# Optimization experiments

Measured on AMD Instinct MI355X. Metric: run time of the kernel, lower is better.

## Reference

```python
import jax, jax.numpy as jnp
import numpy as np

I, H, O = 256, 1024, 256
B, T = 64, 512


def setup_inputs() -> dict:
    key = jax.random.key(0)
    ks = jax.random.split(key, 7)
    s = 1.0 / np.sqrt(H)
    return {
        "x": jax.random.normal(ks[0], (B, T, I), dtype=jnp.float32),
        "W_ih": jax.random.uniform(ks[1], (4 * H, I), jnp.float32, -s, s),
        "W_hh": jax.random.uniform(ks[2], (4 * H, H), jnp.float32, -s, s),
        "b_ih": jax.random.uniform(ks[3], (4 * H,), jnp.float32, -s, s),
        "b_hh": jax.random.uniform(ks[4], (4 * H,), jnp.float32, -s, s),
        "W_out": jax.random.uniform(ks[5], (O, H), jnp.float32, -s, s),
        "b_out": jax.random.uniform(ks[6], (O,), jnp.float32, -s, s),
    }


def _lstm(x, W_ih, W_hh, b_ih, b_hh):
    # Precompute input projection for all timesteps: [B,T,4H]
    xW = jnp.einsum('bti,gi->btg', x, W_ih) + b_ih + b_hh
    Hn = W_hh.shape[1]

    def step(carry, xw_t):
        h, c = carry  # [B,H] each
        z = xw_t + h @ W_hh.T  # [B,4H]
        i = jax.nn.sigmoid(z[:, 0 * Hn:1 * Hn])
        f = jax.nn.sigmoid(z[:, 1 * Hn:2 * Hn])
        g = jnp.tanh(z[:, 2 * Hn:3 * Hn])
        o = jax.nn.sigmoid(z[:, 3 * Hn:4 * Hn])
        c_new = f * c + i * g
        h_new = o * jnp.tanh(c_new)
        return (h_new, c_new), h_new

    h0 = jnp.zeros((x.shape[0], Hn), dtype=x.dtype)
    c0 = jnp.zeros((x.shape[0], Hn), dtype=x.dtype)
    _, hs = jax.lax.scan(step, (h0, c0), jnp.swapaxes(xW, 0, 1))  # hs: [T,B,H]
    return jnp.swapaxes(hs, 0, 1)  # [B,T,H]


def reference(x, W_ih, W_hh, b_ih, b_hh, W_out, b_out):
    h = _lstm(x, W_ih, W_hh, b_ih, b_hh)
    # dropout p=0.0 -> identity; readout_nonlinearity='id'
    y = jnp.einsum('bth,oh->bto', h, W_out) + b_out
    return y
```

## Files before the change

kernel.cpp:

```cpp
#include <hip/hip_runtime.h>

#define NB 64
#define NT 512
#define NI 256
#define NH 1024
#define NO 256
#define NWG 256
#define NU 4
#define NR 16
#define NGRP 16
#define GSZ 16

typedef __attribute__((ext_vector_type(8))) __bf16 bf16x8;
typedef __attribute__((ext_vector_type(8))) unsigned short u16x8;
typedef __attribute__((ext_vector_type(4))) float f32x4;

union FragQ { unsigned long long q[2]; bf16x8 v; };

static __device__ __forceinline__ unsigned short f2bf(float f) {
  unsigned int u = __float_as_uint(f);
  unsigned int r = (u + 0x7fffu + ((u >> 16) & 1u)) >> 16;
  return (unsigned short)r;
}


__global__ void __launch_bounds__(256) xpose_kernel(const float* __restrict__ x,
                                                    unsigned short* __restrict__ xbf,
                                                    unsigned int* __restrict__ bar) {
  if (blockIdx.x == 0 && threadIdx.x < 1 + NGRP)
    __hip_atomic_store(bar + threadIdx.x * 32, 0u, __ATOMIC_RELAXED, __HIP_MEMORY_SCOPE_AGENT);
  int idx = blockIdx.x * 256 + threadIdx.x;
  const int total = NB * NT * NI / 8;
  for (int e = idx; e < total; e += gridDim.x * 256) {
    int i8 = (e & 31) * 8;
    int tb = e >> 5;
    int b = tb & (NB - 1);
    int t = tb >> 6;
    const float* src = x + ((b * NT + t) << 8) + i8;
    u16x8 v;
#pragma unroll
    for (int j = 0; j < 8; ++j) v[j] = f2bf(src[j]);
    *(u16x8*)(xbf + e * 8) = v;
  }
}

__global__ void __launch_bounds__(512) lstm_kernel(
    const unsigned short* __restrict__ xbf,
    const float* __restrict__ Wih,
    const float* __restrict__ Whh,
    const float* __restrict__ bih,
    const float* __restrict__ bhh,
    unsigned short* __restrict__ hall,
    unsigned int* __restrict__ bar) {
  __shared__ __align__(16) unsigned short Wh_l[NR * NH];
  __shared__ __align__(16) unsigned short Wi_l[NR * NI];
  __shared__ float bias_l[NR];
  __shared__ float zbuf[2][NB][17];
  __shared__ __align__(16) unsigned short hstage[NB * NU];

  const int tid = threadIdx.x;
  const int u0 = blockIdx.x * NU;
  const int grp = blockIdx.x >> 4;

  for (int idx = tid; idx < NR * NH; idx += 512) {
    int r = idx >> 10;
    int k = idx & (NH - 1);
    int g = r >> 2, uu = r & 3;
    Wh_l[(r << 10) | (k ^ ((r & 7) << 3))] = f2bf(Whh[(g * NH + u0 + uu) * NH + k]);
  }
  for (int idx = tid; idx < NR * NI; idx += 512) {
    int r = idx >> 8;
    int k = idx & (NI - 1);
    int g = r >> 2, uu = r & 3;
    Wi_l[(r << 8) | (k ^ ((r & 7) << 3))] = f2bf(Wih[(g * NH + u0 + uu) * NI + k]);
  }
  if (tid < NR) {
    int g = tid >> 2, uu = tid & 3;
    bias_l[tid] = bih[g * NH + u0 + uu] + bhh[g * NH + u0 + uu];
  }
  __syncthreads();

  const int wave = tid >> 6;
  const int lane = tid & 63;
  const int lr = lane & 15;
  const int lq = lane >> 4;
  const int m = wave & 3;
  const int kh = wave >> 2;

  const int eb = tid >> 2;
  const int eu = tid & 3;
  float c_state = 0.f;

  const int arow = m * 16 + lr;
  const unsigned short* wi_row = Wi_l + lr * NI;
  const unsigned short* wh_row = Wh_l + lr * NH;
  const int swz = (lr & 7) << 3;

#define COMPUTE_AX(T_, AX0, AX1)                                                \
  do {                                                                          \
    AX0 = (f32x4){0.f, 0.f, 0.f, 0.f};                                          \
    AX1 = (f32x4){0.f, 0.f, 0.f, 0.f};                                          \
    const unsigned short* xrow = xbf + ((T_) * NB + arow) * NI + lq * 8;        \
    _Pragma("unroll")                                                           \
    for (int kk2 = 0; kk2 < 2; ++kk2) {                                         \
      int kk = kh * 4 + kk2 * 2;                                                \
      bf16x8 a0 = *(const bf16x8*)(xrow + kk * 32);                             \
      bf16x8 b0 = *(const bf16x8*)(wi_row + ((kk * 32 + lq * 8) ^ swz));        \
      AX0 = __builtin_amdgcn_mfma_f32_16x16x32_bf16(a0, b0, AX0, 0, 0, 0);      \
      bf16x8 a1 = *(const bf16x8*)(xrow + (kk + 1) * 32);                       \
      bf16x8 b1 = *(const bf16x8*)(wi_row + (((kk + 1) * 32 + lq * 8) ^ swz));  \
      AX1 = __builtin_amdgcn_mfma_f32_16x16x32_bf16(a1, b1, AX1, 0, 0, 0);      \
    }                                                                           \
  } while (0)

  f32x4 ax0, ax1;
  COMPUTE_AX(0, ax0, ax1);

  for (int t = 0; t < NT; ++t) {
    f32x4 ah0 = {0.f, 0.f, 0.f, 0.f};
    f32x4 ah1 = {0.f, 0.f, 0.f, 0.f};
    if (t > 0) {
      const unsigned long long* hrow =
          (const unsigned long long*)(hall + ((t - 1) * NB + arow) * NH) + lq * 2;
#pragma unroll
      for (int kk2 = 0; kk2 < 8; ++kk2) {
        int kk = kh * 16 + kk2 * 2;
        FragQ a0, a1;
        a0.q[0] = hrow[kk * 8 + 0];
        a0.q[1] = hrow[kk * 8 + 1];
        a1.q[0] = hrow[kk * 8 + 8];
        a1.q[1] = hrow[kk * 8 + 9];
        bf16x8 b0 = *(const bf16x8*)(wh_row + ((kk * 32 + lq * 8) ^ swz));
        bf16x8 b1 = *(const bf16x8*)(wh_row + (((kk + 1) * 32 + lq * 8) ^ swz));
        ah0 = __builtin_amdgcn_mfma_f32_16x16x32_bf16(a0.v, b0, ah0, 0, 0, 0);
        ah1 = __builtin_amdgcn_mfma_f32_16x16x32_bf16(a1.v, b1, ah1, 0, 0, 0);
      }
    }
    f32x4 z4 = (ah0 + ah1) + (ax0 + ax1);
#pragma unroll
    for (int j = 0; j < 4; ++j)
      zbuf[kh][m * 16 + lq * 4 + j][lr] = z4[j];
    __syncthreads();

    if (tid < 256) {
      float zi = zbuf[0][eb][0 * NU + eu] + zbuf[1][eb][0 * NU + eu] + bias_l[0 * NU + eu];
      float zf = zbuf[0][eb][1 * NU + eu] + zbuf[1][eb][1 * NU + eu] + bias_l[1 * NU + eu];
      float zg = zbuf[0][eb][2 * NU + eu] + zbuf[1][eb][2 * NU + eu] + bias_l[2 * NU + eu];
      float zo = zbuf[0][eb][3 * NU + eu] + zbuf[1][eb][3 * NU + eu] + bias_l[3 * NU + eu];
      float ig = 1.f / (1.f + __expf(-zi));
      float fg = 1.f / (1.f + __expf(-zf));
      float gg = tanhf(zg);
      float og = 1.f / (1.f + __expf(-zo));
      c_state = fg * c_state + ig * gg;
      float hv = og * tanhf(c_state);
      hstage[eb * NU + eu] = f2bf(hv);
    }
    __syncthreads();

    if (wave == 0) {
      unsigned long long hq = *(const unsigned long long*)(hstage + lane * NU);
      __hip_atomic_store((unsigned long long*)(hall + (t * NB + lane) * NH + u0), hq,
                         __ATOMIC_RELAXED, __HIP_MEMORY_SCOPE_AGENT);
    }
    if (tid == 0) {
      asm volatile("s_waitcnt vmcnt(0)" ::: "memory");
      unsigned int old = __hip_atomic_fetch_add(bar + (grp + 1) * 32, 1u,
                                                __ATOMIC_RELAXED, __HIP_MEMORY_SCOPE_AGENT);
      if (old == (unsigned int)(t * GSZ + (GSZ - 1)))
        __hip_atomic_fetch_add(bar, 1u, __ATOMIC_RELAXED, __HIP_MEMORY_SCOPE_AGENT);
    }
    if (t + 1 < NT) COMPUTE_AX(t + 1, ax0, ax1);
    if (tid == 0) {
      const unsigned int target = (unsigned int)(t + 1) * NGRP;
      while (__hip_atomic_load(bar, __ATOMIC_RELAXED, __HIP_MEMORY_SCOPE_AGENT) < target)
        __builtin_amdgcn_s_sleep(1);
    }
    __syncthreads();
  }
#undef COMPUTE_AX
}

__global__ void __launch_bounds__(256) outproj_kernel(
    const unsigned short* __restrict__ hall,
    const float* __restrict__ Wout,
    const float* __restrict__ bout,
    float* __restrict__ y) {
  __shared__ __align__(16) unsigned short At[64 * 64];
  __shared__ __align__(16) unsigned short Bt[64 * 64];
  const int tid = threadIdx.x;
  const int row0 = blockIdx.x * 64;
  const int col0 = blockIdx.y * 64;
  const int wave = tid >> 6, lane = tid & 63, lr = lane & 15, lq = lane >> 4;
  f32x4 acc[4];
#pragma unroll
  for (int n = 0; n < 4; ++n) acc[n] = (f32x4){0.f, 0.f, 0.f, 0.f};
  const int rr = tid >> 4;
  const int kk4 = (tid & 15) * 4;

  for (int kc = 0; kc < NH / 64; ++kc) {
#pragma unroll
    for (int p = 0; p < 4; ++p) {
      int r = rr + p * 16;
      ushort4 va = *(const ushort4*)(hall + (size_t)(row0 + r) * NH + kc * 64 + kk4);
      *(ushort4*)(At + r * 64 + (kk4 ^ ((r & 7) << 3))) = va;
      float4 vb = *(const float4*)(Wout + (size_t)(col0 + r) * NH + kc * 64 + kk4);
      ushort4 wb;
      wb.x = f2bf(vb.x); wb.y = f2bf(vb.y); wb.z = f2bf(vb.z); wb.w = f2bf(vb.w);
      *(ushort4*)(Bt + r * 64 + (kk4 ^ ((r & 7) << 3))) = wb;
    }
    __syncthreads();
#pragma unroll
    for (int kk = 0; kk < 2; ++kk) {
      int kb = kk * 32 + lq * 8;
      bf16x8 af = *(const bf16x8*)(At + (wave * 16 + lr) * 64 + (kb ^ ((lr & 7) << 3)));
#pragma unroll
      for (int n = 0; n < 4; ++n) {
        bf16x8 bf = *(const bf16x8*)(Bt + (n * 16 + lr) * 64 + (kb ^ ((lr & 7) << 3)));
        acc[n] = __builtin_amdgcn_mfma_f32_16x16x32_bf16(af, bf, acc[n], 0, 0, 0);
      }
    }
    __syncthreads();
  }
#pragma unroll
  for (int n = 0; n < 4; ++n) {
    int o = col0 + n * 16 + lr;
    float bo = bout[o];
#pragma unroll
    for (int j = 0; j < 4; ++j) {
      int r = row0 + wave * 16 + lq * 4 + j;
      int b = r & (NB - 1);
      int t = r >> 6;
      y[(size_t)((b << 9) | t) * NO + o] = acc[n][j] + bo;
    }
  }
}

extern "C" void kernel_launch(void* const* d_in, const int* in_sizes, int n_in,
                              void* d_out, int out_size, void* d_ws, size_t ws_size,
                              hipStream_t stream) {
  const float* x    = (const float*)d_in[0];
  const float* Wih  = (const float*)d_in[1];
  const float* Whh  = (const float*)d_in[2];
  const float* bih  = (const float*)d_in[3];
  const float* bhh  = (const float*)d_in[4];
  const float* Wout = (const float*)d_in[5];
  const float* bout = (const float*)d_in[6];
  float* y = (float*)d_out;

  unsigned short* xbf  = (unsigned short*)d_ws;
  unsigned short* hall = xbf + (size_t)NT * NB * NI;
  unsigned int* bar = (unsigned int*)d_out;

  hipLaunchKernelGGL(xpose_kernel, dim3(1024), dim3(256), 0, stream, x, xbf, bar);

  void* args[7];
  args[0] = (void*)&xbf;
  args[1] = (void*)&Wih;
  args[2] = (void*)&Whh;
  args[3] = (void*)&bih;
  args[4] = (void*)&bhh;
  args[5] = (void*)&hall;
  args[6] = (void*)&bar;
  hipLaunchCooperativeKernel(lstm_kernel, dim3(NWG), dim3(512), args, 0u, stream);

  hipLaunchKernelGGL(outproj_kernel, dim3(512, 4), dim3(256), 0, stream,
                     hall, Wout, bout, y);
}
```

Baseline: 3.612 ms.

## Replace global grid barrier with per-group readiness flags consumed incrementally

Drops the global counter barrier and the end-of-step __syncthreads in the persistent LSTM kernel. Each group's last arriver now publishes a per-group step flag into every consumer's flag row. Each wave polls the flags for its 8 K-chunks and starts MFMAs on whichever hidden-state chunks are already ready, so compute overlaps with straggling producers. The cost is more polling traffic and atomic stores, and ordering now relies on relaxed atomics and the hstage/zbuf reuse without a trailing block barrier.

```diff
diff --git a/kernel.cpp b/kernel.cpp
--- a/kernel.cpp
+++ b/kernel.cpp
@@ -27,8 +27,9 @@
 __global__ void __launch_bounds__(256) xpose_kernel(const float* __restrict__ x,
                                                     unsigned short* __restrict__ xbf,
                                                     unsigned int* __restrict__ bar) {
-  if (blockIdx.x == 0 && threadIdx.x < 1 + NGRP)
-    __hip_atomic_store(bar + threadIdx.x * 32, 0u, __ATOMIC_RELAXED, __HIP_MEMORY_SCOPE_AGENT);
+  if (blockIdx.x == 0)
+    for (int w = threadIdx.x; w < (1 + NGRP * 2) * 32; w += 256)
+      __hip_atomic_store(bar + w, 0u, __ATOMIC_RELAXED, __HIP_MEMORY_SCOPE_AGENT);
   int idx = blockIdx.x * 256 + threadIdx.x;
   const int total = NB * NT * NI / 8;
   for (int e = idx; e < total; e += gridDim.x * 256) {
@@ -95,6 +96,8 @@
   const unsigned short* wi_row = Wi_l + lr * NI;
   const unsigned short* wh_row = Wh_l + lr * NH;
   const int swz = (lr & 7) << 3;
+
+  unsigned int* const flagw = bar + (17 + grp) * 32 + (kh * 8 + (lane & 7));
 
 #define COMPUTE_AX(T_, AX0, AX1)                                                \
   do {                                                                          \
@@ -122,18 +125,27 @@
     if (t > 0) {
       const unsigned long long* hrow =
           (const unsigned long long*)(hall + ((t - 1) * NB + arow) * NH) + lq * 2;
-#pragma unroll
-      for (int kk2 = 0; kk2 < 8; ++kk2) {
-        int kk = kh * 16 + kk2 * 2;
-        FragQ a0, a1;
-        a0.q[0] = hrow[kk * 8 + 0];
-        a0.q[1] = hrow[kk * 8 + 1];
-        a1.q[0] = hrow[kk * 8 + 8];
-        a1.q[1] = hrow[kk * 8 + 9];
-        bf16x8 b0 = *(const bf16x8*)(wh_row + ((kk * 32 + lq * 8) ^ swz));
-        bf16x8 b1 = *(const bf16x8*)(wh_row + (((kk + 1) * 32 + lq * 8) ^ swz));
-        ah0 = __builtin_amdgcn_mfma_f32_16x16x32_bf16(a0.v, b0, ah0, 0, 0, 0);
-        ah1 = __builtin_amdgcn_mfma_f32_16x16x32_bf16(a1.v, b1, ah1, 0, 0, 0);
+      unsigned int done = 0;
+      while (done != 0xffu) {
+        unsigned int f = __hip_atomic_load(flagw, __ATOMIC_RELAXED, __HIP_MEMORY_SCOPE_AGENT);
+        unsigned long long bal = __ballot(f >= (unsigned int)t);
+        unsigned int newm = ((unsigned int)bal & 0xffu) & ~done;
+        if (newm == 0u) { __builtin_amdgcn_s_sleep(1); continue; }
+        done |= newm;
+        do {
+          int g2 = __builtin_ctz(newm);
+          newm &= newm - 1u;
+          int kk = kh * 16 + g2 * 2;
+          FragQ a0, a1;
+          a0.q[0] = hrow[kk * 8 + 0];
+          a0.q[1] = hrow[kk * 8 + 1];
+          a1.q[0] = hrow[kk * 8 + 8];
+          a1.q[1] = hrow[kk * 8 + 9];
+          bf16x8 b0 = *(const bf16x8*)(wh_row + ((kk * 32 + lq * 8) ^ swz));
+          bf16x8 b1 = *(const bf16x8*)(wh_row + (((kk + 1) * 32 + lq * 8) ^ swz));
+          ah0 = __builtin_amdgcn_mfma_f32_16x16x32_bf16(a0.v, b0, ah0, 0, 0, 0);
+          ah1 = __builtin_amdgcn_mfma_f32_16x16x32_bf16(a1.v, b1, ah1, 0, 0, 0);
+        } while (newm);
       }
     }
     f32x4 z4 = (ah0 + ah1) + (ax0 + ax1);
@@ -164,18 +176,16 @@
     }
     if (tid == 0) {
       asm volatile("s_waitcnt vmcnt(0)" ::: "memory");
-      unsigned int old = __hip_atomic_fetch_add(bar + (grp + 1) * 32, 1u,
+      unsigned int old = __hip_atomic_fetch_add(bar + (1 + grp) * 32, 1u,
                                                 __ATOMIC_RELAXED, __HIP_MEMORY_SCOPE_AGENT);
-      if (old == (unsigned int)(t * GSZ + (GSZ - 1)))
-        __hip_atomic_fetch_add(bar, 1u, __ATOMIC_RELAXED, __HIP_MEMORY_SCOPE_AGENT);
+      if (old == (unsigned int)(t * GSZ + (GSZ - 1))) {
+#pragma unroll
+        for (int h = 0; h < NGRP; ++h)
+          __hip_atomic_store(bar + (17 + h) * 32 + grp, (unsigned int)(t + 1),
+                             __ATOMIC_RELAXED, __HIP_MEMORY_SCOPE_AGENT);
+      }
     }
     if (t + 1 < NT) COMPUTE_AX(t + 1, ax0, ax1);
-    if (tid == 0) {
-      const unsigned int target = (unsigned int)(t + 1) * NGRP;
-      while (__hip_atomic_load(bar, __ATOMIC_RELAXED, __HIP_MEMORY_SCOPE_AGENT) < target)
-        __builtin_amdgcn_s_sleep(1);
-    }
-    __syncthreads();
   }
 #undef COMPUTE_AX
 }
```

New measurement: 4.248 ms. +17.6%, slower.
